# Performance work log

Hardware: AMD Instinct MI355X
Metric: run time of the kernel (lower is better)

## Reference

```python
import jax, jax.numpy as jnp
import numpy as np

SEQ_LEN = 20          # hard-coded by the original module's 20x20 DataFrame
SCALE = 1e13          # mse() multiplies by 10000000000000
FRAME_SHAPE = (3, 720, 1280)


def setup_inputs() -> dict:
    key = jax.random.key(0)
    k1, k2 = jax.random.split(key)
    clip1 = jax.random.normal(k1, (SEQ_LEN,) + FRAME_SHAPE, dtype=jnp.float32)
    clip2 = jax.random.normal(k2, (SEQ_LEN,) + FRAME_SHAPE, dtype=jnp.float32)
    return {"clip1": clip1, "clip2": clip2}


def reference(clip1, clip2):
    # M[i, j] = -mean((clip1[j] - clip2[i])**2) * 1e13   (rows = clip2, cols = clip1)
    # Expand the squared difference: mean((a-b)^2) = mean(a^2) + mean(b^2) - 2*mean(a*b)
    # so we never materialize the [n, n, frame] difference tensor.
    n = clip1.shape[0]
    f = clip1[0].size
    c1 = clip1.reshape(n, -1)                       # [n, F]
    c2 = clip2.reshape(n, -1)                       # [n, F]
    m1 = jnp.mean(c1 * c1, axis=1)                  # [n] mean(clip1[j]^2)
    m2 = jnp.mean(c2 * c2, axis=1)                  # [n] mean(clip2[i]^2)
    cross = jnp.einsum('if,jf->ij', c2, c1) / f     # [n, n] mean(clip2[i]*clip1[j])
    M = -(m2[:, None] + m1[None, :] - 2.0 * cross) * SCALE

    # calculate_diagonals_partial: means of diagonals of M at offsets
    # k = -(n//2), ..., -1, 0, 1, ..., n//2 (offset = col - row),
    # each divided by its diagonal length (n - |k|), i.e. a mean.
    half = n // 2
    diags = [jnp.mean(jnp.diagonal(M, offset=k)) for k in range(-half, half + 1)]
    return jnp.stack(diags)                         # [n + 1] = [21]
```

## Files before the change

kernel.cpp:

```cpp
#include <hip/hip_runtime.h>

#define NN      20
#define FF      2764800
#define TK      64
#define NROWS   40
#define NTILES  (FF / TK)
#define NBLK    768
#define NTHREADS 256
#define NW      (NBLK * 4)
#define PAD4    17


__global__ void zero_ws_kernel(float* __restrict__ ws, int n) {
    int i = blockIdx.x * blockDim.x + threadIdx.x;
    if (i < n) ws[i] = 0.0f;
}

__global__ __launch_bounds__(NTHREADS, 3) void gram_kernel(
    const float* __restrict__ clip1,
    const float* __restrict__ clip2,
    float* __restrict__ ws,
    int repMask)
{
    __shared__ float s[4][NROWS * PAD4 * 4];

    const int tid  = threadIdx.x;
    const int lane = tid & 63;
    const int wv   = tid >> 6;
    const int sub  = lane & 15;
    const int kq   = lane >> 4;
    const int gi   = sub >> 2;
    const int gj   = sub & 3;

    float4* const S4 = (float4*)&s[wv][0];

    const float* gp[10];
    float4*      wp[10];
    #pragma unroll
    for (int r = 0; r < 10; ++r) {
        int row = (lane >> 4) + 4 * r;
        const float* base = (row < NN) ? (clip2 + (size_t)row * FF)
                                       : (clip1 + (size_t)(row - NN) * FF);
        gp[r] = base + (lane & 15) * 4;
        wp[r] = S4 + row * PAD4 + (lane & 15);
    }

    const float4* ra[5];
    const float4* rb[5];
    #pragma unroll
    for (int r5 = 0; r5 < 5; ++r5) {
        ra[r5] = S4 + (gi + 4 * r5) * PAD4 + 4 * kq;
        rb[r5] = S4 + (NN + gj + 4 * r5) * PAD4 + 4 * kq;
    }

    float acc[5][5];
    #pragma unroll
    for (int a = 0; a < 5; ++a)
        #pragma unroll
        for (int b = 0; b < 5; ++b) acc[a][b] = 0.0f;
    float sq[10];
    #pragma unroll
    for (int r = 0; r < 10; ++r) sq[r] = 0.0f;

    const int W = blockIdx.x * 4 + wv;
    int t = W;

    float4 v[10];
    #pragma unroll
    for (int r = 0; r < 10; ++r)
        v[r] = *(const float4*)(gp[r] + (size_t)t * TK);

    while (t < NTILES) {
        const int tn = t + NW;

        #pragma unroll
        for (int r = 0; r < 10; ++r) {
            *wp[r] = v[r];
            sq[r] += v[r].x * v[r].x + v[r].y * v[r].y
                   + v[r].z * v[r].z + v[r].w * v[r].w;
        }

        if (tn < NTILES) {
            #pragma unroll
            for (int r = 0; r < 10; ++r)
                v[r] = *(const float4*)(gp[r] + (size_t)tn * TK);
        }

        #pragma unroll
        for (int q = 0; q < 4; ++q) {
            float4 a5[5], b5[5];
            #pragma unroll
            for (int x = 0; x < 5; ++x) { a5[x] = ra[x][q]; b5[x] = rb[x][q]; }
            #pragma unroll
            for (int ri = 0; ri < 5; ++ri)
                #pragma unroll
                for (int rj = 0; rj < 5; ++rj) {
                    acc[ri][rj] += a5[ri].x * b5[rj].x;
                    acc[ri][rj] += a5[ri].y * b5[rj].y;
                    acc[ri][rj] += a5[ri].z * b5[rj].z;
                    acc[ri][rj] += a5[ri].w * b5[rj].w;
                }
        }
        t = tn;
    }

    float* wsr = ws + (blockIdx.x & repMask) * 440;

    #pragma unroll
    for (int a = 0; a < 5; ++a)
        #pragma unroll
        for (int b = 0; b < 5; ++b) {
            float vsum = acc[a][b];
            vsum += __shfl_down(vsum, 32);
            vsum += __shfl_down(vsum, 16);
            acc[a][b] = vsum;
        }

    __syncthreads();
    float* red = &s[0][0];
    if (lane < 16) {
        #pragma unroll
        for (int a = 0; a < 5; ++a)
            #pragma unroll
            for (int b = 0; b < 5; ++b)
                red[(wv * 16 + lane) * 25 + a * 5 + b] = acc[a][b];
    }
    __syncthreads();

    for (int p = tid; p < 400; p += NTHREADS) {
        int psub = p / 25;
        int rem  = p % 25;
        int pa   = rem / 5;
        int pb   = rem % 5;
        float vsum = red[(0 * 16 + psub) * 25 + rem]
                   + red[(1 * 16 + psub) * 25 + rem]
                   + red[(2 * 16 + psub) * 25 + rem]
                   + red[(3 * 16 + psub) * 25 + rem];
        int i = (psub >> 2) + 4 * pa;
        int j = (psub & 3) + 4 * pb;
        atomicAdd(&wsr[i * NN + j], vsum);
    }

    #pragma unroll
    for (int r = 0; r < 10; ++r) {
        float vq = sq[r];
        vq += __shfl_xor(vq, 8);
        vq += __shfl_xor(vq, 4);
        vq += __shfl_xor(vq, 2);
        vq += __shfl_xor(vq, 1);
        if ((lane & 15) == 0) {
            int row = (lane >> 4) + 4 * r;
            atomicAdd(&wsr[400 + row], vq);
        }
    }
}

__global__ void finalize_kernel(const float* __restrict__ ws, float* __restrict__ out,
                                int nrep) {
    int d = threadIdx.x;
    if (d >= 21) return;
    int k  = d - 10;
    int a  = k < 0 ? -k : k;
    int i0 = k < 0 ? -k : 0;
    int L  = NN - a;
    const float invF = 1.0f / (float)FF;
    float sum = 0.0f;
    for (int m = 0; m < L; ++m) {
        int i = i0 + m;
        int j = i + k;
        float q2 = 0.f, q1 = 0.f, cr = 0.f;
        for (int rep = 0; rep < nrep; ++rep) {
            const float* w = ws + rep * 440;
            q2 += w[400 + i];
            q1 += w[420 + j];
            cr += w[i * NN + j];
        }
        sum += q2 + q1 - 2.0f * cr;
    }
    out[d] = -(sum * invF / (float)L) * 1e13f;
}

extern "C" void kernel_launch(void* const* d_in, const int* in_sizes, int n_in,
                              void* d_out, int out_size, void* d_ws, size_t ws_size,
                              hipStream_t stream) {
    const float* clip1 = (const float*)d_in[0];
    const float* clip2 = (const float*)d_in[1];
    float* out = (float*)d_out;
    float* ws  = (float*)d_ws;

    int nrep = 1;
    while (nrep < 16 && (size_t)(nrep * 2) * 440 * sizeof(float) <= ws_size)
        nrep *= 2;

    int nz = nrep * 440;
    zero_ws_kernel<<<(nz + 255) / 256, 256, 0, stream>>>(ws, nz);
    gram_kernel<<<NBLK, NTHREADS, 0, stream>>>(clip1, clip2, ws, nrep - 1);
    finalize_kernel<<<1, 64, 0, stream>>>(ws, out, nrep);
}
```

Baseline: 141.0 us.

## Compute Gram matrix with bf16 MFMA and async global-to-LDS double buffering

Replaces the scalar FMA 5x5 register-tile Gram computation with 16x16x32 bf16 MFMA instructions. Each of the four waves owns one 16x16 output tile. Tiles are streamed via global_load_lds into a swizzled, double-buffered shared array, with more blocks and more atomic replica slots. Converting inputs to bf16 introduces precision loss in the cross term, which is then amplified by the 1e13 scale and by cancellation in a^2+b^2-2ab. This risks numerical mismatch, while the goal is to relieve the FMA-bound compute so the kernel reaches the memory-bandwidth limit.

```diff
diff --git a/kernel.cpp b/kernel.cpp
--- a/kernel.cpp
+++ b/kernel.cpp
@@ -1,14 +1,15 @@
 #include <hip/hip_runtime.h>
+#include <hip/hip_bf16.h>
 
 #define NN      20
 #define FF      2764800
 #define TK      64
-#define NROWS   40
 #define NTILES  (FF / TK)
-#define NBLK    768
+#define NBLK    1792
 #define NTHREADS 256
-#define NW      (NBLK * 4)
-#define PAD4    17
+
+typedef __attribute__((ext_vector_type(8))) short bf16x8;
+typedef __attribute__((ext_vector_type(4))) float f32x4;
 
 
 __global__ void zero_ws_kernel(float* __restrict__ ws, int n) {
@@ -16,142 +17,128 @@
     if (i < n) ws[i] = 0.0f;
 }
 
-__global__ __launch_bounds__(NTHREADS, 3) void gram_kernel(
+static __device__ inline float sq4(float4 v) {
+    return v.x * v.x + v.y * v.y + v.z * v.z + v.w * v.w;
+}
+
+static __device__ inline bf16x8 cvt8(float4 lo, float4 hi) {
+    union { __hip_bfloat162 h[4]; bf16x8 v; } u;
+    u.h[0] = __float22bfloat162_rn(float2{lo.x, lo.y});
+    u.h[1] = __float22bfloat162_rn(float2{lo.z, lo.w});
+    u.h[2] = __float22bfloat162_rn(float2{hi.x, hi.y});
+    u.h[3] = __float22bfloat162_rn(float2{hi.z, hi.w});
+    return u.v;
+}
+
+__global__ __launch_bounds__(NTHREADS, 7) void gram_kernel(
     const float* __restrict__ clip1,
     const float* __restrict__ clip2,
     float* __restrict__ ws,
     int repMask)
 {
-    __shared__ float s[4][NROWS * PAD4 * 4];
+    __shared__ __align__(16) float s[2][40 * TK];
 
     const int tid  = threadIdx.x;
     const int lane = tid & 63;
     const int wv   = tid >> 6;
-    const int sub  = lane & 15;
+    const int sidx = lane & 15;
     const int kq   = lane >> 4;
-    const int gi   = sub >> 2;
-    const int gj   = sub & 3;
+    const int ti   = wv >> 1;
+    const int tj   = wv & 1;
 
-    float4* const S4 = (float4*)&s[wv][0];
-
-    const float* gp[10];
-    float4*      wp[10];
+    const int nq = (wv < 2) ? 3 : 2;
+    const float* gbase[3];
+    unsigned voff[3];
+    int lq[3];
     #pragma unroll
-    for (int r = 0; r < 10; ++r) {
-        int row = (lane >> 4) + 4 * r;
-        const float* base = (row < NN) ? (clip2 + (size_t)row * FF)
-                                       : (clip1 + (size_t)(row - NN) * FF);
-        gp[r] = base + (lane & 15) * 4;
-        wp[r] = S4 + row * PAD4 + (lane & 15);
+    for (int k = 0; k < 3; ++k) {
+        int q   = wv + 4 * k;
+        lq[k]   = q;
+        int row = 4 * q + kq;
+        int mm  = sidx ^ (row & 7);
+        int rl  = (row < NN) ? row : row - NN;
+        gbase[k] = (row < NN) ? clip2 : clip1;
+        voff[k]  = (unsigned)rl * FF + (unsigned)mm * 4;
     }
 
-    const float4* ra[5];
-    const float4* rb[5];
+    const int rowA = ti * 16 + sidx;
+    const int rowB = 20 + tj * 16 + (tj ? (sidx < 4 ? sidx : 3) : sidx);
+    const int swzA = rowA & 7;
+    const int swzB = rowB & 7;
+
+    f32x4 acc = {0.f, 0.f, 0.f, 0.f};
+    float sqa = 0.f, sqb = 0.f;
+
+    int t = blockIdx.x;
     #pragma unroll
-    for (int r5 = 0; r5 < 5; ++r5) {
-        ra[r5] = S4 + (gi + 4 * r5) * PAD4 + 4 * kq;
-        rb[r5] = S4 + (NN + gj + 4 * r5) * PAD4 + 4 * kq;
+    for (int k = 0; k < 3; ++k) {
+        if (k < nq) {
+            const float* ga = gbase[k] + (size_t)voff[k] + (size_t)t * TK;
+            char* la = (char*)&s[0][0] + lq[k] * 1024;
+            __builtin_amdgcn_global_load_lds(
+                (const __attribute__((address_space(1))) void*)ga,
+                (__attribute__((address_space(3))) void*)la, 16, 0, 0);
+        }
     }
+    __syncthreads();
 
-    float acc[5][5];
-    #pragma unroll
-    for (int a = 0; a < 5; ++a)
-        #pragma unroll
-        for (int b = 0; b < 5; ++b) acc[a][b] = 0.0f;
-    float sq[10];
-    #pragma unroll
-    for (int r = 0; r < 10; ++r) sq[r] = 0.0f;
-
-    const int W = blockIdx.x * 4 + wv;
-    int t = W;
-
-    float4 v[10];
-    #pragma unroll
-    for (int r = 0; r < 10; ++r)
-        v[r] = *(const float4*)(gp[r] + (size_t)t * TK);
-
+    int cur = 0;
     while (t < NTILES) {
-        const int tn = t + NW;
-
-        #pragma unroll
-        for (int r = 0; r < 10; ++r) {
-            *wp[r] = v[r];
-            sq[r] += v[r].x * v[r].x + v[r].y * v[r].y
-                   + v[r].z * v[r].z + v[r].w * v[r].w;
+        const int tn = t + NBLK;
+        if (tn < NTILES) {
+            #pragma unroll
+            for (int k = 0; k < 3; ++k) {
+                if (k < nq) {
+                    const float* ga = gbase[k] + (size_t)voff[k] + (size_t)tn * TK;
+                    char* la = (char*)&s[cur ^ 1][0] + lq[k] * 1024;
+                    __builtin_amdgcn_global_load_lds(
+                        (const __attribute__((address_space(1))) void*)ga,
+                        (__attribute__((address_space(3))) void*)la, 16, 0, 0);
+                }
+            }
         }
 
-        if (tn < NTILES) {
-            #pragma unroll
-            for (int r = 0; r < 10; ++r)
-                v[r] = *(const float4*)(gp[r] + (size_t)tn * TK);
+        const float* buf = &s[cur][0];
+        #pragma unroll
+        for (int ch = 0; ch < 2; ++ch) {
+            const int bA = 8 * ch + 2 * kq;
+            float4 a0 = *(const float4*)&buf[rowA * TK + (((bA    ) ^ swzA) << 2)];
+            float4 a1 = *(const float4*)&buf[rowA * TK + (((bA + 1) ^ swzA) << 2)];
+            float4 b0 = *(const float4*)&buf[rowB * TK + (((bA    ) ^ swzB) << 2)];
+            float4 b1 = *(const float4*)&buf[rowB * TK + (((bA + 1) ^ swzB) << 2)];
+            if (tj == 0) sqa += sq4(a0) + sq4(a1);
+            if (ti == 0) sqb += sq4(b0) + sq4(b1);
+            acc = __builtin_amdgcn_mfma_f32_16x16x32_bf16(
+                      cvt8(a0, a1), cvt8(b0, b1), acc, 0, 0, 0);
         }
 
-        #pragma unroll
-        for (int q = 0; q < 4; ++q) {
-            float4 a5[5], b5[5];
-            #pragma unroll
-            for (int x = 0; x < 5; ++x) { a5[x] = ra[x][q]; b5[x] = rb[x][q]; }
-            #pragma unroll
-            for (int ri = 0; ri < 5; ++ri)
-                #pragma unroll
-                for (int rj = 0; rj < 5; ++rj) {
-                    acc[ri][rj] += a5[ri].x * b5[rj].x;
-                    acc[ri][rj] += a5[ri].y * b5[rj].y;
-                    acc[ri][rj] += a5[ri].z * b5[rj].z;
-                    acc[ri][rj] += a5[ri].w * b5[rj].w;
-                }
-        }
+        __syncthreads();
+        cur ^= 1;
         t = tn;
     }
 
     float* wsr = ws + (blockIdx.x & repMask) * 440;
 
     #pragma unroll
-    for (int a = 0; a < 5; ++a)
-        #pragma unroll
-        for (int b = 0; b < 5; ++b) {
-            float vsum = acc[a][b];
-            vsum += __shfl_down(vsum, 32);
-            vsum += __shfl_down(vsum, 16);
-            acc[a][b] = vsum;
-        }
-
-    __syncthreads();
-    float* red = &s[0][0];
-    if (lane < 16) {
-        #pragma unroll
-        for (int a = 0; a < 5; ++a)
-            #pragma unroll
-            for (int b = 0; b < 5; ++b)
-                red[(wv * 16 + lane) * 25 + a * 5 + b] = acc[a][b];
-    }
-    __syncthreads();
-
-    for (int p = tid; p < 400; p += NTHREADS) {
-        int psub = p / 25;
-        int rem  = p % 25;
-        int pa   = rem / 5;
-        int pb   = rem % 5;
-        float vsum = red[(0 * 16 + psub) * 25 + rem]
-                   + red[(1 * 16 + psub) * 25 + rem]
-                   + red[(2 * 16 + psub) * 25 + rem]
-                   + red[(3 * 16 + psub) * 25 + rem];
-        int i = (psub >> 2) + 4 * pa;
-        int j = (psub & 3) + 4 * pb;
-        atomicAdd(&wsr[i * NN + j], vsum);
+    for (int r = 0; r < 4; ++r) {
+        int i = ti * 16 + kq * 4 + r;
+        int j = tj * 16 + sidx;
+        if (i < NN && j < NN) atomicAdd(&wsr[i * NN + j], acc[r]);
     }
 
-    #pragma unroll
-    for (int r = 0; r < 10; ++r) {
-        float vq = sq[r];
-        vq += __shfl_xor(vq, 8);
-        vq += __shfl_xor(vq, 4);
-        vq += __shfl_xor(vq, 2);
-        vq += __shfl_xor(vq, 1);
-        if ((lane & 15) == 0) {
-            int row = (lane >> 4) + 4 * r;
-            atomicAdd(&wsr[400 + row], vq);
-        }
+    float va = sqa;
+    va += __shfl_xor(va, 16);
+    va += __shfl_xor(va, 32);
+    if (tj == 0 && kq == 0) {
+        int i = ti * 16 + sidx;
+        if (i < NN) atomicAdd(&wsr[400 + i], va);
+    }
+    float vb = sqb;
+    vb += __shfl_xor(vb, 16);
+    vb += __shfl_xor(vb, 32);
+    if (ti == 0 && kq == 0) {
+        int j = tj * 16 + sidx;
+        if (j < NN) atomicAdd(&wsr[420 + j], vb);
     }
 }
 
@@ -189,7 +176,7 @@
     float* ws  = (float*)d_ws;
 
     int nrep = 1;
-    while (nrep < 16 && (size_t)(nrep * 2) * 440 * sizeof(float) <= ws_size)
+    while (nrep < 64 && (size_t)(nrep * 2) * 440 * sizeof(float) <= ws_size)
         nrep *= 2;
 
     int nz = nrep * 440;
```

After: 286.4 us. 103% more time.
